# Kernel optimization log

Measured on AMD Instinct MI355X. Metric: run time of the kernel, lower is better.

Reference implementation:

```python
import jax, jax.numpy as jnp
import numpy as np

B, T, D, H, C = 2, 2048, 256, 8, 2
HEAD = C * D  # per-head embedding size = num_channels * dim(irreps)


def setup_inputs() -> dict:
    key = jax.random.key(0)
    ks = jax.random.split(key, 8)
    n = lambda k, shape, scale=1.0: jax.random.normal(k, shape, jnp.float32) * scale
    return {
        "q": n(ks[0], (B, T, D)),
        "k": n(ks[1], (B, T, D)),
        "v": n(ks[2], (B, T, D)),
        "mask": jnp.ones((B, 1, T, T), dtype=bool),  # [..., H=1, T', T], broadcast over heads
        "Wq": n(ks[3], (D, H * HEAD), 1.0 / np.sqrt(D)),
        "Wk": n(ks[4], (D, H * HEAD), 1.0 / np.sqrt(D)),
        "Wv": n(ks[5], (D, H * HEAD), 1.0 / np.sqrt(D)),
        "Wo": n(ks[6], (H * HEAD, HEAD), 1.0 / np.sqrt(H * HEAD)),
    }


def reference(q, k, v, mask, Wq, Wk, Wv, Wo):
    # Linear projections (e3nn Linear on scalar irreps == bias-free dense),
    # then mul_to_axis(num_heads, axis=-2): [B,T,H*C*D] -> [B,T,H,C*D]
    qh = (q @ Wq).reshape(B, T, H, HEAD)
    kh = (k @ Wk).reshape(B, T, H, HEAD)
    vh = (v @ Wv).reshape(B, T, H, HEAD)

    scale = 1.0 / jnp.sqrt(jnp.asarray(HEAD, qh.dtype))
    logits = jnp.einsum("bthd,bThd->bhtT", qh, kh) * scale  # [B,H,T,T]
    logits = jnp.where(mask, logits, jnp.asarray(-1e30, logits.dtype))
    w = jax.nn.softmax(logits, axis=-1)

    attn = jnp.einsum("bhtT,bThd->bthd", w, vh)  # [B,T,H,HEAD]
    attn = attn.reshape(B, T, H * HEAD)  # axis_to_mul(axis=-2): merge heads
    return attn @ Wo  # final Linear to num_channels*irreps -> [B,T,HEAD]
```

## Files before the change

kernel.cpp:

```cpp
#include <hip/hip_runtime.h>
#include <hip/hip_bf16.h>
#include <stdint.h>

typedef __hip_bfloat16 bf16;
typedef __bf16 v8bf __attribute__((ext_vector_type(8)));
typedef float v4f __attribute__((ext_vector_type(4)));


__global__ __launch_bounds__(256)
void detect_f32(const uint16_t* __restrict__ q, uint32_t* __restrict__ flag)
{
  const int tid = threadIdx.x;
  float m = 0.f;
#pragma unroll
  for (int i = 0; i < 8; ++i) {
    uint32_t u = (uint32_t)q[tid * 8 + i] << 16;
    float x;
    __builtin_memcpy(&x, &u, 4);
    x = fabsf(x);
    if (!(x <= 1e30f)) x = 1e30f;
    m = fmaxf(m, x);
  }
#pragma unroll
  for (int o = 32; o > 0; o >>= 1) m = fmaxf(m, __shfl_xor(m, o));
  __shared__ float red[4];
  if ((tid & 63) == 0) red[tid >> 6] = m;
  __syncthreads();
  if (tid == 0) {
    m = fmaxf(fmaxf(red[0], red[1]), fmaxf(red[2], red[3]));
    flag[0] = (m > 1e4f) ? 1u : 0u;
    flag[1] = 0u;
  }
}

__global__ __launch_bounds__(256)
void convert3_bf16(const void* __restrict__ in0, const void* __restrict__ in1,
                   const void* __restrict__ in2, bf16* __restrict__ out,
                   const uint32_t* __restrict__ flag)
{
  const void* in = (blockIdx.y == 0) ? in0 : (blockIdx.y == 1) ? in1 : in2;
  bf16* o = out + (size_t)blockIdx.y * 1048576;
  const int i = (blockIdx.x * 256 + threadIdx.x) * 4;
  if (flag[0]) {
    const float4 f = *(const float4*)((const float*)in + i);
    union { uint2 u; bf16 b[4]; } ob;
    ob.b[0] = __float2bfloat16(f.x);
    ob.b[1] = __float2bfloat16(f.y);
    ob.b[2] = __float2bfloat16(f.z);
    ob.b[3] = __float2bfloat16(f.w);
    *(uint2*)(o + i) = ob.u;
  } else {
    *(uint2*)(o + i) = *(const uint2*)((const bf16*)in + i);
  }
}

__global__ __launch_bounds__(256)
void transpose_all(const void* __restrict__ w0, const void* __restrict__ w1,
                   const void* __restrict__ w2, const void* __restrict__ wo,
                   bf16* __restrict__ outW, bf16* __restrict__ outWo,
                   const uint32_t* __restrict__ flag)
{
  const int z = blockIdx.z;
  const void* in;
  bf16* o;
  int ldin, ldout, bx32, by32;
  if (z < 3) {
    if (blockIdx.y >= 8) return;
    in = (z == 0) ? w0 : (z == 1) ? w1 : w2;
    o = outW + (size_t)z * 1048576;
    ldin = 4096; ldout = 256;
    bx32 = blockIdx.x * 32;
    by32 = blockIdx.y * 32;
  } else {
    in = wo; o = outWo;
    ldin = 512; ldout = 4096;
    bx32 = blockIdx.y * 32;
    by32 = blockIdx.x * 32;
  }
  __shared__ float tile[32][33];
  const int r  = threadIdx.x >> 3;
  const int c4 = (threadIdx.x & 7) * 4;
  const bool isf = (flag[0] != 0);
#pragma unroll
  for (int j = 0; j < 4; ++j) {
    const long idx = (long)(by32 + r) * ldin + bx32 + c4 + j;
    tile[r][c4 + j] = isf ? ((const float*)in)[idx]
                          : __bfloat162float(((const bf16*)in)[idx]);
  }
  __syncthreads();
#pragma unroll
  for (int j = 0; j < 4; ++j)
    o[(size_t)(bx32 + r) * ldout + by32 + c4 + j] = __float2bfloat16(tile[c4 + j][r]);
}

__device__ __forceinline__ void gld_lds16(const bf16* g, bf16* l) {
  __builtin_amdgcn_global_load_lds(
      (const __attribute__((address_space(1))) void*)g,
      (__attribute__((address_space(3))) void*)l, 16, 0, 0);
}

template <int MODE>
__global__ __launch_bounds__(256)
void gemm_tpl(const bf16* __restrict__ A, const bf16* __restrict__ Bt,
              void* __restrict__ Cv, int K, int lda, int ldb, int ldc,
              long sA, long sB, long sC)
{
  A  += (long)blockIdx.z * sA;
  Bt += (long)blockIdx.z * sB;
  bf16* Cb = (bf16*)Cv + (long)blockIdx.z * sC;

  const int m0 = blockIdx.x * 128;
  const int n0 = blockIdx.y * 128;
  const int tid  = threadIdx.x;
  const int lane = tid & 63;
  const int wave = tid >> 6;
  const int wr   = (wave >> 1) * 64;
  const int wc   = (wave & 1) * 64;
  const int l16  = lane & 15;
  const int quad = lane >> 4;

  __shared__ __align__(16) bf16 As0[4096], As1[4096], Bs0[4096], Bs1[4096];

  v4f acc[4][4];
#pragma unroll
  for (int i = 0; i < 4; ++i)
#pragma unroll
    for (int j = 0; j < 4; ++j) acc[i][j] = (v4f){0.f, 0.f, 0.f, 0.f};

  const int srow = tid >> 2;
  const int scol = (tid & 3) * 8;

  for (int k0 = 0; k0 < K; k0 += 64) {
    const bf16* Ab = A  + (size_t)(m0 + srow) * lda + k0 + scol;
    const bf16* Bb = Bt + (size_t)(n0 + srow) * ldb + k0 + scol;
    gld_lds16(Ab,                      As0 + tid * 8);
    gld_lds16(Ab + (size_t)64 * lda,   As0 + 2048 + tid * 8);
    gld_lds16(Ab + 32,                 As1 + tid * 8);
    gld_lds16(Ab + (size_t)64 * lda + 32, As1 + 2048 + tid * 8);
    gld_lds16(Bb,                      Bs0 + tid * 8);
    gld_lds16(Bb + (size_t)64 * ldb,   Bs0 + 2048 + tid * 8);
    gld_lds16(Bb + 32,                 Bs1 + tid * 8);
    gld_lds16(Bb + (size_t)64 * ldb + 32, Bs1 + 2048 + tid * 8);
    __syncthreads();

    v8bf af[4], bfr[4];
#pragma unroll
    for (int i = 0; i < 4; ++i) {
      af[i]  = *(const v8bf*)&As0[(wr + i * 16 + l16) * 32 + quad * 8];
      bfr[i] = *(const v8bf*)&Bs0[(wc + i * 16 + l16) * 32 + quad * 8];
    }
#pragma unroll
    for (int i = 0; i < 4; ++i)
#pragma unroll
      for (int j = 0; j < 4; ++j)
        acc[i][j] = __builtin_amdgcn_mfma_f32_16x16x32_bf16(af[i], bfr[j], acc[i][j], 0, 0, 0);

#pragma unroll
    for (int i = 0; i < 4; ++i) {
      af[i]  = *(const v8bf*)&As1[(wr + i * 16 + l16) * 32 + quad * 8];
      bfr[i] = *(const v8bf*)&Bs1[(wc + i * 16 + l16) * 32 + quad * 8];
    }
#pragma unroll
    for (int i = 0; i < 4; ++i)
#pragma unroll
      for (int j = 0; j < 4; ++j)
        acc[i][j] = __builtin_amdgcn_mfma_f32_16x16x32_bf16(af[i], bfr[j], acc[i][j], 0, 0, 0);
    __syncthreads();
  }

#pragma unroll
  for (int i = 0; i < 4; ++i) {
    const int r0 = m0 + wr + i * 16 + quad * 4;
#pragma unroll
    for (int j = 0; j < 4; ++j) {
      const int cc = n0 + wc + j * 16 + l16;
#pragma unroll
      for (int r = 0; r < 4; ++r)
        Cb[(size_t)(r0 + r) * ldc + cc] = __float2bfloat16(acc[i][j][r]);
    }
  }
}

__global__ __launch_bounds__(256)
void gemm_pv(const bf16* __restrict__ Sb, const bf16* __restrict__ VWT,
             bf16* __restrict__ attnO, const float* __restrict__ rsPart)
{
  const int id = blockIdx.x;
  const int h  = id & 7;
  const int j  = id >> 3;
  const int m0 = (j >> 2) * 128;
  const int n0 = (j & 3) * 128;
  const bf16* A  = Sb  + (size_t)h * 4194304;
  const bf16* Bt = VWT + (size_t)h * 1048576;
  bf16* Cb = attnO + (size_t)h * 1048576;
  const float* rsp = rsPart + (size_t)h * 8 * 2048;

  const int tid  = threadIdx.x;
  const int lane = tid & 63;
  const int wave = tid >> 6;
  const int wr   = (wave >> 1) * 64;
  const int wc   = (wave & 1) * 64;
  const int l16  = lane & 15;
  const int quad = lane >> 4;

  __shared__ __align__(16) bf16 As0[4096], As1[4096], Bs0[4096], Bs1[4096];

  v4f acc[4][4];
#pragma unroll
  for (int i = 0; i < 4; ++i)
#pragma unroll
    for (int j2 = 0; j2 < 4; ++j2) acc[i][j2] = (v4f){0.f, 0.f, 0.f, 0.f};

  const int srow = tid >> 2;
  const int scol = (tid & 3) * 8;

  for (int k0 = 0; k0 < 2048; k0 += 64) {
    const bf16* Ab = A  + (size_t)(m0 + srow) * 2048 + k0 + scol;
    const bf16* Bb = Bt + (size_t)(n0 + srow) * 2048 + k0 + scol;
    gld_lds16(Ab,                       As0 + tid * 8);
    gld_lds16(Ab + (size_t)64 * 2048,   As0 + 2048 + tid * 8);
    gld_lds16(Ab + 32,                  As1 + tid * 8);
    gld_lds16(Ab + (size_t)64 * 2048 + 32, As1 + 2048 + tid * 8);
    gld_lds16(Bb,                       Bs0 + tid * 8);
    gld_lds16(Bb + (size_t)64 * 2048,   Bs0 + 2048 + tid * 8);
    gld_lds16(Bb + 32,                  Bs1 + tid * 8);
    gld_lds16(Bb + (size_t)64 * 2048 + 32, Bs1 + 2048 + tid * 8);
    __syncthreads();

    v8bf af[4], bfr[4];
#pragma unroll
    for (int i = 0; i < 4; ++i) {
      af[i]  = *(const v8bf*)&As0[(wr + i * 16 + l16) * 32 + quad * 8];
      bfr[i] = *(const v8bf*)&Bs0[(wc + i * 16 + l16) * 32 + quad * 8];
    }
#pragma unroll
    for (int i = 0; i < 4; ++i)
#pragma unroll
      for (int j2 = 0; j2 < 4; ++j2)
        acc[i][j2] = __builtin_amdgcn_mfma_f32_16x16x32_bf16(af[i], bfr[j2], acc[i][j2], 0, 0, 0);

#pragma unroll
    for (int i = 0; i < 4; ++i) {
      af[i]  = *(const v8bf*)&As1[(wr + i * 16 + l16) * 32 + quad * 8];
      bfr[i] = *(const v8bf*)&Bs1[(wc + i * 16 + l16) * 32 + quad * 8];
    }
#pragma unroll
    for (int i = 0; i < 4; ++i)
#pragma unroll
      for (int j2 = 0; j2 < 4; ++j2)
        acc[i][j2] = __builtin_amdgcn_mfma_f32_16x16x32_bf16(af[i], bfr[j2], acc[i][j2], 0, 0, 0);
    __syncthreads();
  }

#pragma unroll
  for (int i = 0; i < 4; ++i) {
    const int r0 = m0 + wr + i * 16 + quad * 4;
    float inv[4];
#pragma unroll
    for (int r = 0; r < 4; ++r) {
      float s = 0.f;
#pragma unroll
      for (int t8 = 0; t8 < 8; ++t8) s += rsp[t8 * 2048 + r0 + r];
      inv[r] = 1.0f / s;
    }
#pragma unroll
    for (int j2 = 0; j2 < 4; ++j2) {
      const int cc = n0 + wc + j2 * 16 + l16;
#pragma unroll
      for (int r = 0; r < 4; ++r)
        Cb[(size_t)(r0 + r) * 512 + cc] = __float2bfloat16(acc[i][j2][r] * inv[r]);
    }
  }
}

__global__ __launch_bounds__(256, 2)
void gemm_s256(const bf16* __restrict__ A0, const bf16* __restrict__ Bt0,
               bf16* __restrict__ C0, float scale, float* __restrict__ rsPart)
{
  const int id = blockIdx.x;
  const int z  = id & 7;
  const int j  = id >> 3;
  const int m0 = (j >> 3) * 128;
  const int nt = j & 7;
  const int n0 = nt * 256;
  const bf16* A  = A0  + (size_t)z * 512;
  const bf16* Bt = Bt0 + (size_t)z * 512;
  bf16* C = C0 + (size_t)z * 4194304;

  const int tid  = threadIdx.x;
  const int lane = tid & 63;
  const int wave = tid >> 6;
  const int wr   = (wave >> 1) * 64;
  const int wc   = (wave & 1) * 128;
  const int l16  = lane & 15;
  const int quad = lane >> 4;

  __shared__ __align__(16) bf16 As0[4096], As1[4096];
  __shared__ __align__(16) bf16 Bs0[8192], Bs1[8192];
  __shared__ float rsLds[2][128];

  v4f acc[4][8];
#pragma unroll
  for (int i = 0; i < 4; ++i)
#pragma unroll
    for (int jj = 0; jj < 8; ++jj) acc[i][jj] = (v4f){0.f, 0.f, 0.f, 0.f};

  const int srow = tid >> 2;
  const int scol = (tid & 3) * 8;

  for (int k0 = 0; k0 < 512; k0 += 64) {
    const bf16* Ab = A  + (size_t)(m0 + srow) * 4096 + k0 + scol;
    const bf16* Bb = Bt + (size_t)(n0 + srow) * 4096 + k0 + scol;
    gld_lds16(Ab,                        As0 + tid * 8);
    gld_lds16(Ab + (size_t)64 * 4096,    As0 + 2048 + tid * 8);
    gld_lds16(Ab + 32,                   As1 + tid * 8);
    gld_lds16(Ab + (size_t)64 * 4096 + 32, As1 + 2048 + tid * 8);
#pragma unroll
    for (int s = 0; s < 4; ++s) {
      gld_lds16(Bb + (size_t)(s * 64) * 4096,      Bs0 + s * 2048 + tid * 8);
      gld_lds16(Bb + (size_t)(s * 64) * 4096 + 32, Bs1 + s * 2048 + tid * 8);
    }
    __syncthreads();

#pragma unroll
    for (int sub = 0; sub < 2; ++sub) {
      const bf16* Asx = sub ? As1 : As0;
      const bf16* Bsx = sub ? Bs1 : Bs0;
      v8bf af[4];
#pragma unroll
      for (int i = 0; i < 4; ++i)
        af[i] = *(const v8bf*)&Asx[(wr + i * 16 + l16) * 32 + quad * 8];
#pragma unroll
      for (int jg = 0; jg < 2; ++jg) {
        v8bf bf4[4];
#pragma unroll
        for (int j4 = 0; j4 < 4; ++j4)
          bf4[j4] = *(const v8bf*)&Bsx[(wc + jg * 64 + j4 * 16 + l16) * 32 + quad * 8];
#pragma unroll
        for (int i = 0; i < 4; ++i)
#pragma unroll
          for (int j4 = 0; j4 < 4; ++j4)
            acc[i][jg * 4 + j4] =
                __builtin_amdgcn_mfma_f32_16x16x32_bf16(af[i], bf4[j4], acc[i][jg * 4 + j4], 0, 0, 0);
      }
    }
    __syncthreads();
  }

#pragma unroll
  for (int i = 0; i < 4; ++i) {
    const int lr0 = wr + i * 16 + quad * 4;
    float rsm[4] = {0.f, 0.f, 0.f, 0.f};
#pragma unroll
    for (int jj = 0; jj < 8; ++jj) {
      const int cc = n0 + wc + jj * 16 + l16;
#pragma unroll
      for (int r = 0; r < 4; ++r) {
        float e = __expf(acc[i][jj][r] * scale);
        bf16 pb = __float2bfloat16(e);
        C[(size_t)(m0 + lr0 + r) * 2048 + cc] = pb;
        rsm[r] += __bfloat162float(pb);
      }
    }
#pragma unroll
    for (int r = 0; r < 4; ++r) {
      float s = rsm[r];
      s += __shfl_xor(s, 1); s += __shfl_xor(s, 2);
      s += __shfl_xor(s, 4); s += __shfl_xor(s, 8);
      if (l16 == 0) rsLds[wave & 1][lr0 + r] = s;
    }
  }
  __syncthreads();
  if (tid < 128)
    rsPart[((size_t)z * 8 + nt) * 2048 + m0 + tid] = rsLds[0][tid] + rsLds[1][tid];
}

__global__ __launch_bounds__(256)
void reduce8(const bf16* __restrict__ attnO, void* __restrict__ out,
             long outOff, const uint32_t* __restrict__ flag)
{
  const int i = (blockIdx.x * 256 + threadIdx.x) * 8;
  float s[8] = {0.f, 0.f, 0.f, 0.f, 0.f, 0.f, 0.f, 0.f};
#pragma unroll
  for (int h = 0; h < 8; ++h) {
    uint4 u = *(const uint4*)(attnO + (size_t)h * 1048576 + i);
    const bf16* bb = (const bf16*)&u;
#pragma unroll
    for (int r = 0; r < 8; ++r) s[r] += __bfloat162float(bb[r]);
  }
  if (flag[0]) {
    float* op = (float*)out + outOff + i;
    *(float4*)op       = (float4){s[0], s[1], s[2], s[3]};
    *(float4*)(op + 4) = (float4){s[4], s[5], s[6], s[7]};
  } else {
    union { uint4 u; bf16 b[8]; } o;
#pragma unroll
    for (int r = 0; r < 8; ++r) o.b[r] = __float2bfloat16(s[r]);
    *(uint4*)((bf16*)out + outOff + i) = o.u;
  }
}

extern "C" void kernel_launch(void* const* d_in, const int* in_sizes, int n_in,
                              void* d_out, int out_size, void* d_ws, size_t ws_size,
                              hipStream_t stream)
{
  const void* q  = d_in[0];
  const void* k  = d_in[1];
  const void* v  = d_in[2];
  const void* Wq = d_in[4];
  const void* Wk = d_in[5];
  const void* Wv = d_in[6];
  const void* Wo = d_in[7];

  char* base = (char*)d_ws;
  size_t off = 0;
  auto alloc = [&](size_t bytes) -> char* {
    char* p = base + off;
    off = (off + bytes + 255) & ~(size_t)255;
    return p;
  };
  uint32_t* flag = (uint32_t*)alloc(256);
  bf16* qc  = (bf16*)alloc(2097152);
  bf16* kc  = (bf16*)alloc(2097152);
  bf16* vc  = (bf16*)alloc(2097152);
  bf16* WqT = (bf16*)alloc(2097152);
  bf16* WkT = (bf16*)alloc(2097152);
  bf16* WvT = (bf16*)alloc(2097152);
  bf16* WoT = (bf16*)alloc(4194304);
  bf16*  qh   = (bf16*)alloc(50331648);
  bf16*  VWT  = (bf16*)alloc(16777216);
  bf16*  Sbuf = (bf16*)alloc(67108864);
  float* rsPart = (float*)alloc(524288);
  bf16* kh = qh + 8388608;
  bf16* vh = qh + 16777216;
  bf16* attnO = qh;

  const dim3 blk(256);
  const float scale = 0.04419417382415922f;

  detect_f32<<<1, blk, 0, stream>>>((const uint16_t*)q, flag);
  convert3_bf16<<<dim3(1024, 3), blk, 0, stream>>>(q, k, v, qc, flag);
  transpose_all<<<dim3(128, 16, 4), blk, 0, stream>>>(Wq, Wk, Wv, Wo, WqT, WoT, flag);

  for (int b = 0; b < 2; ++b) {
    const bf16* xb = qc + (size_t)b * 524288;

    gemm_tpl<0><<<dim3(16, 32, 3), blk, 0, stream>>>(
        xb, WqT, qh, 256, 256, 256, 4096,
        1048576, 1048576, 8388608);

    gemm_tpl<0><<<dim3(4, 16, 8), blk, 0, stream>>>(
        WoT, vh, VWT, 512, 4096, 4096, 2048,
        512, 512, 1048576);

    gemm_s256<<<dim3(1024), blk, 0, stream>>>(qh, kh, Sbuf, scale, rsPart);

    gemm_pv<<<dim3(512), blk, 0, stream>>>(Sbuf, VWT, attnO, rsPart);

    reduce8<<<dim3(512), blk, 0, stream>>>(attnO, d_out, (long)b * 1048576, flag);
  }
}
```

Measured before the change: 382.4 us.

## Fuse dtype detection into convert and batch projection GEMMs across batch

Result: faster. 363.0 us (-5.1%).

```diff
diff --git a/kernel.cpp b/kernel.cpp
--- a/kernel.cpp
+++ b/kernel.cpp
@@ -8,13 +8,21 @@
 
 
 __global__ __launch_bounds__(256)
-void detect_f32(const uint16_t* __restrict__ q, uint32_t* __restrict__ flag)
-{
+void convert3_bf16(const void* __restrict__ in0, const void* __restrict__ in1,
+                   const void* __restrict__ in2, bf16* __restrict__ out,
+                   uint32_t* __restrict__ flag)
+{
+  const void* in = (blockIdx.y == 0) ? in0 : (blockIdx.y == 1) ? in1 : in2;
+  bf16* o = out + (size_t)blockIdx.y * 1048576;
   const int tid = threadIdx.x;
+  const int i = (blockIdx.x * 256 + tid) * 4;
+
+  uint2 raw = *(const uint2*)((const uint16_t*)in + i);
+  const uint16_t* hw = (const uint16_t*)&raw;
   float m = 0.f;
 #pragma unroll
-  for (int i = 0; i < 8; ++i) {
-    uint32_t u = (uint32_t)q[tid * 8 + i] << 16;
+  for (int r = 0; r < 4; ++r) {
+    uint32_t u = (uint32_t)hw[r] << 16;
     float x;
     __builtin_memcpy(&x, &u, 4);
     x = fabsf(x);
@@ -22,26 +30,14 @@
     m = fmaxf(m, x);
   }
 #pragma unroll
-  for (int o = 32; o > 0; o >>= 1) m = fmaxf(m, __shfl_xor(m, o));
+  for (int off = 32; off > 0; off >>= 1) m = fmaxf(m, __shfl_xor(m, off));
   __shared__ float red[4];
   if ((tid & 63) == 0) red[tid >> 6] = m;
   __syncthreads();
-  if (tid == 0) {
-    m = fmaxf(fmaxf(red[0], red[1]), fmaxf(red[2], red[3]));
-    flag[0] = (m > 1e4f) ? 1u : 0u;
-    flag[1] = 0u;
-  }
-}
-
-__global__ __launch_bounds__(256)
-void convert3_bf16(const void* __restrict__ in0, const void* __restrict__ in1,
-                   const void* __restrict__ in2, bf16* __restrict__ out,
-                   const uint32_t* __restrict__ flag)
-{
-  const void* in = (blockIdx.y == 0) ? in0 : (blockIdx.y == 1) ? in1 : in2;
-  bf16* o = out + (size_t)blockIdx.y * 1048576;
-  const int i = (blockIdx.x * 256 + threadIdx.x) * 4;
-  if (flag[0]) {
+  const bool isf = fmaxf(fmaxf(red[0], red[1]), fmaxf(red[2], red[3])) > 1e4f;
+  if (blockIdx.x == 0 && blockIdx.y == 0 && tid == 0) flag[0] = isf ? 1u : 0u;
+
+  if (isf) {
     const float4 f = *(const float4*)((const float*)in + i);
     union { uint2 u; bf16 b[4]; } ob;
     ob.b[0] = __float2bfloat16(f.x);
@@ -50,7 +46,7 @@
     ob.b[3] = __float2bfloat16(f.w);
     *(uint2*)(o + i) = ob.u;
   } else {
-    *(uint2*)(o + i) = *(const uint2*)((const bf16*)in + i);
+    *(uint2*)(o + i) = raw;
   }
 }
 
@@ -103,11 +99,14 @@
 __global__ __launch_bounds__(256)
 void gemm_tpl(const bf16* __restrict__ A, const bf16* __restrict__ Bt,
               void* __restrict__ Cv, int K, int lda, int ldb, int ldc,
-              long sA, long sB, long sC)
-{
-  A  += (long)blockIdx.z * sA;
-  Bt += (long)blockIdx.z * sB;
-  bf16* Cb = (bf16*)Cv + (long)blockIdx.z * sC;
+              int zsh, long sAlo, long sAhi, long sBlo, long sBhi,
+              long sClo, long sChi)
+{
+  const int zlo = blockIdx.z & ((1 << zsh) - 1);
+  const int zhi = blockIdx.z >> zsh;
+  A  += (long)zlo * sAlo + (long)zhi * sAhi;
+  Bt += (long)zlo * sBlo + (long)zhi * sBhi;
+  bf16* Cb = (bf16*)Cv + (long)zlo * sClo + (long)zhi * sChi;
 
   const int m0 = blockIdx.x * 128;
   const int n0 = blockIdx.y * 128;
@@ -421,42 +420,53 @@
   };
   uint32_t* flag = (uint32_t*)alloc(256);
   bf16* qc  = (bf16*)alloc(2097152);
-  bf16* kc  = (bf16*)alloc(2097152);
-  bf16* vc  = (bf16*)alloc(2097152);
+  bf16* kc  = (bf16*)alloc(2097152);  (void)kc;
+  bf16* vc  = (bf16*)alloc(2097152);  (void)vc;
   bf16* WqT = (bf16*)alloc(2097152);
-  bf16* WkT = (bf16*)alloc(2097152);
-  bf16* WvT = (bf16*)alloc(2097152);
+  bf16* WkT = (bf16*)alloc(2097152);  (void)WkT;
+  bf16* WvT = (bf16*)alloc(2097152);  (void)WvT;
   bf16* WoT = (bf16*)alloc(4194304);
-  bf16*  qh   = (bf16*)alloc(50331648);
-  bf16*  VWT  = (bf16*)alloc(16777216);
+
+  const size_t needB = 100663296ULL + 33554432ULL + 67108864ULL + 524288ULL + 4096ULL;
+  const bool big = (ws_size > off) && (ws_size - off >= needB);
+
+  bf16*  qh   = (bf16*)alloc(big ? 100663296 : 50331648);
+  bf16*  VWT  = (bf16*)alloc(big ? 33554432 : 16777216);
   bf16*  Sbuf = (bf16*)alloc(67108864);
   float* rsPart = (float*)alloc(524288);
-  bf16* kh = qh + 8388608;
-  bf16* vh = qh + 16777216;
-  bf16* attnO = qh;
 
   const dim3 blk(256);
   const float scale = 0.04419417382415922f;
-
-  detect_f32<<<1, blk, 0, stream>>>((const uint16_t*)q, flag);
+  const long qhB = 25165824;
+
   convert3_bf16<<<dim3(1024, 3), blk, 0, stream>>>(q, k, v, qc, flag);
   transpose_all<<<dim3(128, 16, 4), blk, 0, stream>>>(Wq, Wk, Wv, Wo, WqT, WoT, flag);
 
-  for (int b = 0; b < 2; ++b) {
-    const bf16* xb = qc + (size_t)b * 524288;
-
-    gemm_tpl<0><<<dim3(16, 32, 3), blk, 0, stream>>>(
-        xb, WqT, qh, 256, 256, 256, 4096,
-        1048576, 1048576, 8388608);
-
-    gemm_tpl<0><<<dim3(4, 16, 8), blk, 0, stream>>>(
-        WoT, vh, VWT, 512, 4096, 4096, 2048,
-        512, 512, 1048576);
-
-    gemm_s256<<<dim3(1024), blk, 0, stream>>>(qh, kh, Sbuf, scale, rsPart);
-
-    gemm_pv<<<dim3(512), blk, 0, stream>>>(Sbuf, VWT, attnO, rsPart);
-
-    reduce8<<<dim3(512), blk, 0, stream>>>(attnO, d_out, (long)b * 1048576, flag);
-  }
-}
+  if (big) {
+    gemm_tpl<0><<<dim3(16, 32, 6), blk, 0, stream>>>(
+        qc, WqT, qh, 256, 256, 256, 4096,
+        1, 524288, 1048576, 0, 1048576, qhB, 8388608);
+    gemm_tpl<0><<<dim3(4, 16, 16), blk, 0, stream>>>(
+        WoT, qh + 16777216, VWT, 512, 4096, 4096, 2048,
+        3, 512, 0, 512, qhB, 1048576, 8388608);
+    for (int b = 0; b < 2; ++b) {
+      bf16* qhb = qh + (size_t)b * qhB;
+      gemm_s256<<<dim3(1024), blk, 0, stream>>>(qhb, qhb + 8388608, Sbuf, scale, rsPart);
+      gemm_pv<<<dim3(512), blk, 0, stream>>>(Sbuf, VWT + (size_t)b * 8388608, qhb, rsPart);
+      reduce8<<<dim3(512), blk, 0, stream>>>(qhb, d_out, (long)b * 1048576, flag);
+    }
+  } else {
+    for (int b = 0; b < 2; ++b) {
+      const bf16* xb = qc + (size_t)b * 524288;
+      gemm_tpl<0><<<dim3(16, 32, 3), blk, 0, stream>>>(
+          xb, WqT, qh, 256, 256, 256, 4096,
+          0, 0, 1048576, 0, 1048576, 0, 8388608);
+      gemm_tpl<0><<<dim3(4, 16, 8), blk, 0, stream>>>(
+          WoT, qh + 16777216, VWT, 512, 4096, 4096, 2048,
+          0, 0, 512, 0, 512, 0, 1048576);
+      gemm_s256<<<dim3(1024), blk, 0, stream>>>(qh, qh + 8388608, Sbuf, scale, rsPart);
+      gemm_pv<<<dim3(512), blk, 0, stream>>>(Sbuf, VWT, qh, rsPart);
+      reduce8<<<dim3(512), blk, 0, stream>>>(qh, d_out, (long)b * 1048576, flag);
+    }
+  }
+}
```
